# Kernel tuning notes

Hardware: AMD Instinct MI355X
Metric: run time of the kernel (lower is better)

## Reference

```python
import jax, jax.numpy as jnp
import numpy as np

B, CIN, COUT, DK, DV, NH, H, W = 8, 256, 512, 256, 256, 8, 32, 32
DKH = DK // NH  # 32
DVH = DV // NH  # 32


def _conv(x, w, b, pad):
    y = jax.lax.conv_general_dilated(
        x, w, window_strides=(1, 1), padding=[(pad, pad), (pad, pad)],
        dimension_numbers=('NCHW', 'OIHW', 'NCHW'))
    return y + b[None, :, None, None]


def setup_inputs() -> dict:
    key = jax.random.key(0)
    ks = jax.random.split(key, 6)
    s = jnp.float32(0.05)
    return {
        'x': jax.random.normal(ks[0], (B, CIN, H, W), jnp.float32),
        'w_conv': jax.random.normal(ks[1], (COUT - DV, CIN, 3, 3), jnp.float32) * s,
        'b_conv': jnp.zeros((COUT - DV,), jnp.float32),
        'w_qkv': jax.random.normal(ks[2], (2 * DK + DV, CIN, 3, 3), jnp.float32) * s,
        'b_qkv': jnp.zeros((2 * DK + DV,), jnp.float32),
        'w_att': jax.random.normal(ks[3], (DV, DV, 1, 1), jnp.float32) * s,
        'b_att': jnp.zeros((DV,), jnp.float32),
        'key_rel_w': jax.random.normal(ks[4], (2 * W - 1, DKH), jnp.float32),
        'key_rel_h': jax.random.normal(ks[5], (2 * H - 1, DKH), jnp.float32),
    }


def reference(x, w_conv, b_conv, w_qkv, b_qkv, w_att, b_att, key_rel_w, key_rel_h):
    qkv = _conv(x, w_qkv, b_qkv, 1)                 # (B, 2*DK+DV, H, W)
    b = x.shape[0]
    q, k, v = qkv[:, :DK], qkv[:, DK:2 * DK], qkv[:, 2 * DK:]
    q = q.reshape(b, NH, DKH, H, W) * (DKH ** -0.5)
    kf = k.reshape(b, NH, DKH, H * W)
    vf = v.reshape(b, NH, DVH, H * W)
    qf = q.reshape(b, NH, DKH, H * W)
    # content logits: (B, NH, HW, HW)
    logits = jnp.einsum('bhdm,bhdn->bhmn', qf, kf)
    # relative position logits (equivalent to the pad/reshape/slice skew trick)
    q5 = jnp.transpose(q, (0, 1, 3, 4, 2))          # (B, NH, H, W, DKH)
    rel_w = jnp.einsum('bhxyd,md->bhxym', q5, key_rel_w)   # (B,NH,H,W,2W-1)
    idx_w = (jnp.arange(W)[None, :] - jnp.arange(W)[:, None]) + (W - 1)  # idx[y,y']
    rel_w = jnp.take_along_axis(rel_w, idx_w[None, None, None], axis=-1)  # (B,NH,H,W,W) [x,y,y']
    rel_h = jnp.einsum('bhxyd,md->bhxym', q5, key_rel_h)   # (B,NH,H,W,2H-1)
    idx_h = (jnp.arange(H)[None, :] - jnp.arange(H)[:, None]) + (H - 1)  # idx[x,x']
    rel_h = jnp.take_along_axis(rel_h, idx_h[None, None, :, None, :], axis=-1)  # (B,NH,H,W,H) [x,y,x']
    # logits6 axes: [x, y, x', y']
    logits6 = (logits.reshape(b, NH, H, W, H, W)
               + rel_w[:, :, :, :, None, :]
               + rel_h[:, :, :, :, :, None])
    weights = jax.nn.softmax(logits6.reshape(b, NH, H * W, H * W), axis=-1)
    att = jnp.einsum('bhmn,bhdn->bhmd', weights, vf)  # (B, NH, HW, DVH)
    # faithful to torch's contiguous .view(batch, dim_v, H, W)
    att = att.reshape(b, DV, H, W)
    att = _conv(att, w_att, b_att, 0)
    xo = _conv(x, w_conv, b_conv, 1)
    return jnp.concatenate([xo, att], axis=1)
```

## Files before the change

kernel.cpp:

```cpp
#include <hip/hip_runtime.h>


typedef __attribute__((ext_vector_type(8))) short short8;
typedef __attribute__((ext_vector_type(4))) float floatx4;

__device__ __forceinline__ unsigned short f2bf(float f) {
    unsigned int u = __float_as_uint(f);
    u += 0x7FFFu + ((u >> 16) & 1u);
    return (unsigned short)(u >> 16);
}
__device__ __forceinline__ float bf2f(unsigned short s) {
    return __uint_as_float(((unsigned int)s) << 16);
}
__device__ __forceinline__ unsigned int pk2bf_trunc(float lo, float hi) {
    return (__float_as_uint(lo) >> 16) | (__float_as_uint(hi) & 0xFFFF0000u);
}
__device__ __forceinline__ unsigned int pk2bf_rne(float lo, float hi) {
    return (unsigned int)f2bf(lo) | ((unsigned int)f2bf(hi) << 16);
}
__device__ __forceinline__ void gload_lds16(const unsigned short* g, unsigned short* s) {
    __builtin_amdgcn_global_load_lds(
        (const __attribute__((address_space(1))) unsigned int*)g,
        (__attribute__((address_space(3))) unsigned int*)s, 16, 0, 0);
}

__global__ __launch_bounds__(256) void k_xt(const float* __restrict__ x,
                                            unsigned short* __restrict__ Xt) {
    __shared__ unsigned short lds[256 * 33];
    const int tid = threadIdx.x;
    const int yy = blockIdx.x % 34;
    const int b  = blockIdx.x / 34;
    unsigned int* outp = (unsigned int*)(Xt + (((size_t)b * 34 + yy) * 34) * 256);
    if (yy == 0 || yy == 33) {
        for (int i = tid; i < 4352; i += 256) outp[i] = 0;
        return;
    }
    const int y = yy - 1;
    const float* xb = x + (size_t)b * 262144 + y * 32;
#pragma unroll
    for (int it = 0; it < 32; ++it) {
        const int e = it * 256 + tid;
        const int ci = e >> 5, xx = e & 31;
        lds[ci * 33 + xx] = f2bf(xb[ci * 1024 + xx]);
    }
    __syncthreads();
    const int ci2 = (tid & 127) * 2;
    const int xh = tid >> 7;
#pragma unroll
    for (int it = 0; it < 17; ++it) {
        const int xx = xh * 17 + it;
        unsigned int v = 0;
        if (xx >= 1 && xx <= 32)
            v = (unsigned int)lds[ci2 * 33 + xx - 1] |
                ((unsigned int)lds[(ci2 + 1) * 33 + xx - 1] << 16);
        outp[xx * 128 + (tid & 127)] = v;
    }
}

__global__ __launch_bounds__(256) void k_wconv(const float* __restrict__ wc,
                                               const float* __restrict__ wq,
                                               const float* __restrict__ wa,
                                               const float* __restrict__ krw,
                                               const float* __restrict__ krh,
                                               unsigned short* __restrict__ wt,
                                               unsigned short* __restrict__ wt2,
                                               unsigned short* __restrict__ krwb,
                                               unsigned short* __restrict__ krhb) {
    const int tid = threadIdx.x;
    const int blk = blockIdx.x;
    if (blk < 1024) {
        __shared__ float lw[2304];
        const int n = blk;
        const float* src = (n < 256) ? (wc + (size_t)n * 2304)
                                     : (wq + (size_t)(n - 256) * 2304);
#pragma unroll
        for (int it = 0; it < 9; ++it)
            lw[it * 256 + tid] = src[it * 256 + tid];
        __syncthreads();
#pragma unroll
        for (int it = 0; it < 9; ++it) {
            const int kp = it * 256 + tid;
            const int g = kp >> 8, ci = kp & 255;
            wt[(size_t)n * 2304 + kp] = f2bf(lw[ci * 9 + g]);
        }
    } else {
        const int i = (blk - 1024) * 256 + tid;
        if (i < 65536)        wt2[i] = f2bf(wa[i]);
        else if (i < 67584) { const int j = i - 65536;
                              krwb[j] = (j < 2016) ? f2bf(krw[j]) : (unsigned short)0; }
        else if (i < 69632) { const int j = i - 67584;
                              krhb[j] = (j < 2016) ? f2bf(krh[j]) : (unsigned short)0; }
    }
}

__global__ __launch_bounds__(256, 4) void k_gemm0(const unsigned short* __restrict__ Wr,
                                                  const unsigned short* __restrict__ Xt,
                                                  float* __restrict__ out,
                                                  unsigned short* __restrict__ qT,
                                                  unsigned short* __restrict__ kT,
                                                  unsigned short* __restrict__ vT,
                                                  const float* __restrict__ bias_a,
                                                  const float* __restrict__ bias_b) {
    __shared__ unsigned short As[64 * 64];
    __shared__ unsigned short Bs[128 * 64];
    const int tid = threadIdx.x;
    const int lane = tid & 63, wv = tid >> 6;
    const int l15 = lane & 15, quad = lane >> 4;
    const int m0 = blockIdx.x * 128, n0 = blockIdx.y * 64;
    const int wave_m = (wv & 1) * 64, wave_n = (wv >> 1) * 32;
    floatx4 acc[2][4] = {};
    const int lr = lane >> 3;
    const int swz8 = ((lane & 7) ^ lr) * 8;
    const unsigned short* gA = Wr + (size_t)(n0 + wv * 16 + lr) * 2304 + swz8;
    int bb0[4];
#pragma unroll
    for (int r = 0; r < 4; ++r) {
        const int m = m0 + wv * 32 + r * 8 + lr;
        const int b = m >> 10, p = m & 1023, y = p >> 5, x = p & 31;
        bb0[r] = ((b * 34 + y) * 34 + x) * 256;
    }
    unsigned short* sA0 = As + wv * 1024;
    unsigned short* sB0 = Bs + wv * 2048;
    const int sw0 = ((quad)     ^ (l15 & 7)) * 8;
    const int sw1 = ((4 + quad) ^ (l15 & 7)) * 8;
    for (int k0 = 0; k0 < 2304; k0 += 64) {
        const int g = k0 >> 8;
        const int ci0 = k0 & 255;
        const int ky = g / 3, kx = g - ky * 3;
        const int offu = (ky * 34 + kx) * 256 + ci0 + swz8;
        __syncthreads();
        gload_lds16(gA + k0, sA0);
        gload_lds16(gA + (size_t)8 * 2304 + k0, sA0 + 512);
#pragma unroll
        for (int r = 0; r < 4; ++r)
            gload_lds16(Xt + bb0[r] + offu, sB0 + r * 512);
        __syncthreads();
#pragma unroll
        for (int h = 0; h < 2; ++h) {
            const int sw = h ? sw1 : sw0;
            short8 a[2], b[4];
#pragma unroll
            for (int i = 0; i < 2; ++i)
                a[i] = *reinterpret_cast<const short8*>(As + (wave_n + i * 16 + l15) * 64 + sw);
#pragma unroll
            for (int j = 0; j < 4; ++j)
                b[j] = *reinterpret_cast<const short8*>(Bs + (wave_m + j * 16 + l15) * 64 + sw);
#pragma unroll
            for (int i = 0; i < 2; ++i)
#pragma unroll
                for (int j = 0; j < 4; ++j)
                    acc[i][j] = __builtin_amdgcn_mfma_f32_16x16x32_bf16(a[i], b[j], acc[i][j], 0, 0, 0);
        }
    }
#pragma unroll
    for (int i = 0; i < 2; ++i)
#pragma unroll
        for (int jj = 0; jj < 4; ++jj)
#pragma unroll
            for (int rg = 0; rg < 4; ++rg) {
                const int n = n0 + wave_n + i * 16 + quad * 4 + rg;
                const int m = m0 + wave_m + jj * 16 + l15;
                const float v = acc[i][jj][rg];
                const int bb = m >> 10, p = m & 1023;
                if (n < 256) {
                    out[(size_t)bb * 524288 + (size_t)n * 1024 + p] = v + bias_a[n];
                } else {
                    const int c = n - 256;
                    const float vq = v + bias_b[c];
                    if (c < 256) {
                        const int h = c >> 5, d = c & 31;
                        qT[(((size_t)(bb * 8 + h)) * 1024 + p) * 32 + d] =
                            f2bf(vq * 0.17677669529663687f);
                    } else if (c < 512) {
                        const int c2 = c - 256;
                        const int h = c2 >> 5, d = c2 & 31;
                        kT[(((size_t)(bb * 8 + h)) * 1024 + p) * 32 + d] = f2bf(vq);
                    } else {
                        const int c2 = c - 512;
                        const int h = c2 >> 5, d = c2 & 31;
                        vT[(((size_t)(bb * 8 + h)) * 32 + d) * 1024 + p] = f2bf(vq);
                    }
                }
            }
}

__global__ __launch_bounds__(256, 4) void k_attn(const unsigned short* __restrict__ qT,
                                                 const unsigned short* __restrict__ kT,
                                                 const unsigned short* __restrict__ vT,
                                                 const unsigned short* __restrict__ krwb,
                                                 const unsigned short* __restrict__ krhb,
                                                 unsigned short* __restrict__ attT) {
    __shared__ float rh_s[64 * 68];
    __shared__ unsigned short Pw[4 * 1152];
    const int tid = threadIdx.x;
    const int lane = tid & 63, wv = tid >> 6;
    const int l15 = lane & 15, quad = lane >> 4;
    const int bid = blockIdx.x;
    const int qt = bid & 15;
    const int h = (bid >> 4) & 7;
    const int b = bid >> 7;
    const int bh = b * 8 + h;
    const unsigned short* qbase = qT + (size_t)bh * 32768;
    const unsigned short* kbase = kT + (size_t)bh * 32768;
    const unsigned short* vbase = vT + (size_t)bh * 32768;
    const int qloc = wv * 16 + l15;
    const int pq = qt * 64 + qloc;
    const int yq = pq >> 5, xq = pq & 31;

    const short8 qfrag = *reinterpret_cast<const short8*>(
        qbase + (size_t)pq * 32 + quad * 8);
    const floatx4 zero = {0.f, 0.f, 0.f, 0.f};
    unsigned short* pw = Pw + wv * 1152;

#pragma unroll
    for (int sub = 0; sub < 4; ++sub) {
        const short8 aw = *reinterpret_cast<const short8*>(krwb + (sub * 16 + l15) * 32 + quad * 8);
        const short8 ah = *reinterpret_cast<const short8*>(krhb + (sub * 16 + l15) * 32 + quad * 8);
        const floatx4 dw = __builtin_amdgcn_mfma_f32_16x16x32_bf16(aw, qfrag, zero, 0, 0, 0);
        const floatx4 dh = __builtin_amdgcn_mfma_f32_16x16x32_bf16(ah, qfrag, zero, 0, 0, 0);
        *reinterpret_cast<floatx4*>(rh_s + qloc * 68 + sub * 16 + quad * 4) = dh;
        uint2 uu;
        uu.x = pk2bf_rne(dw[0], dw[1]);
        uu.y = pk2bf_rne(dw[2], dw[3]);
        *reinterpret_cast<uint2*>(pw + l15 * 64 + sub * 16 + quad * 4) = uu;
    }
    float rwreg[8];
#pragma unroll
    for (int j = 0; j < 8; ++j) {
        const int xn = (j >> 2) * 16 + quad * 4 + (j & 3);
        rwreg[j] = bf2f(pw[l15 * 64 + xn - xq + 31]);
    }
    asm volatile("s_waitcnt lgkmcnt(0)" ::: "memory");

    const float* rhq = rh_s + qloc * 68 + 31 - yq;
    float lsum = 0.f;
    floatx4 O0 = zero, O1 = zero;

    short8 kf[4], vf[4];
#pragma unroll
    for (int sub = 0; sub < 4; ++sub)
        kf[sub] = *reinterpret_cast<const short8*>(
            kbase + (size_t)(sub * 16 + l15) * 32 + quad * 8);
#pragma unroll
    for (int n2 = 0; n2 < 2; ++n2) {
        vf[n2 * 2 + 0] = *reinterpret_cast<const short8*>(
            vbase + (size_t)l15 * 1024 + n2 * 32 + quad * 8);
        vf[n2 * 2 + 1] = *reinterpret_cast<const short8*>(
            vbase + (size_t)(16 + l15) * 1024 + n2 * 32 + quad * 8);
    }

#pragma unroll
    for (int nt = 0; nt < 16; ++nt) {
        const int n0 = nt * 64;
        const int n0n = (nt < 15) ? n0 + 64 : n0;
        floatx4 d[4];
#pragma unroll
        for (int sub = 0; sub < 4; ++sub)
            d[sub] = __builtin_amdgcn_mfma_f32_16x16x32_bf16(kf[sub], qfrag, zero, 0, 0, 0);
        short8 kfn[4], vfn[4];
#pragma unroll
        for (int sub = 0; sub < 4; ++sub)
            kfn[sub] = *reinterpret_cast<const short8*>(
                kbase + (size_t)(n0n + sub * 16 + l15) * 32 + quad * 8);
        const float rh0 = rhq[nt * 2];
        const float rh1 = rhq[nt * 2 + 1];
        float p[16];
#pragma unroll
        for (int sub = 0; sub < 4; ++sub) {
            const float rhv = (sub >> 1) ? rh1 : rh0;
#pragma unroll
            for (int r = 0; r < 4; ++r) {
                const float e = __expf(d[sub][r] + rwreg[(sub & 1) * 4 + r] + rhv);
                p[sub * 4 + r] = e;
                lsum += e;
            }
        }
#pragma unroll
        for (int sub = 0; sub < 4; ++sub) {
            uint2 uu;
            uu.x = pk2bf_trunc(p[sub * 4 + 0], p[sub * 4 + 1]);
            uu.y = pk2bf_trunc(p[sub * 4 + 2], p[sub * 4 + 3]);
            *reinterpret_cast<uint2*>(pw + l15 * 72 + sub * 16 + quad * 4) = uu;
        }
        asm volatile("s_waitcnt lgkmcnt(0)" ::: "memory");
#pragma unroll
        for (int n2 = 0; n2 < 2; ++n2) {
            const short8 pfrag = *reinterpret_cast<const short8*>(
                pw + l15 * 72 + n2 * 32 + quad * 8);
            O0 = __builtin_amdgcn_mfma_f32_16x16x32_bf16(vf[n2 * 2 + 0], pfrag, O0, 0, 0, 0);
            O1 = __builtin_amdgcn_mfma_f32_16x16x32_bf16(vf[n2 * 2 + 1], pfrag, O1, 0, 0, 0);
        }
#pragma unroll
        for (int n2 = 0; n2 < 2; ++n2) {
            vfn[n2 * 2 + 0] = *reinterpret_cast<const short8*>(
                vbase + (size_t)l15 * 1024 + n0n + n2 * 32 + quad * 8);
            vfn[n2 * 2 + 1] = *reinterpret_cast<const short8*>(
                vbase + (size_t)(16 + l15) * 1024 + n0n + n2 * 32 + quad * 8);
        }
#pragma unroll
        for (int i = 0; i < 4; ++i) { kf[i] = kfn[i]; vf[i] = vfn[i]; }
    }
    lsum += __shfl_xor(lsum, 16);
    lsum += __shfl_xor(lsum, 32);
    const float inv = 1.0f / lsum;
    unsigned short* ob = attT + ((size_t)(h * 32 + yq)) * 8192 + b * 1024 + xq * 32;
    uint2 o0, o1;
    o0.x = pk2bf_rne(O0[0] * inv, O0[1] * inv);
    o0.y = pk2bf_rne(O0[2] * inv, O0[3] * inv);
    o1.x = pk2bf_rne(O1[0] * inv, O1[1] * inv);
    o1.y = pk2bf_rne(O1[2] * inv, O1[3] * inv);
    *reinterpret_cast<uint2*>(ob + quad * 4) = o0;
    *reinterpret_cast<uint2*>(ob + 16 + quad * 4) = o1;
}

__global__ __launch_bounds__(256) void k_tr(const unsigned short* __restrict__ src,
                                            unsigned short* __restrict__ dst) {
    __shared__ unsigned short t[64 * 72];
    const int tid = threadIdx.x;
    const int m0 = (blockIdx.x & 127) * 64;
    const int k0 = (blockIdx.x >> 7) * 64;
#pragma unroll
    for (int i = 0; i < 2; ++i) {
        const int idx = i * 256 + tid;
        const int k = idx >> 3, c8 = (idx & 7) * 8;
        *reinterpret_cast<uint4*>(t + k * 72 + c8) =
            *reinterpret_cast<const uint4*>(src + (size_t)(k0 + k) * 8192 + m0 + c8);
    }
    __syncthreads();
#pragma unroll
    for (int i = 0; i < 2; ++i) {
        const int idx = i * 256 + tid;
        const int m = idx >> 3, c8 = (idx & 7) * 8;
        unsigned short v[8];
#pragma unroll
        for (int j = 0; j < 8; ++j) v[j] = t[(c8 + j) * 72 + m];
        *reinterpret_cast<uint4*>(dst + (size_t)(m0 + m) * 256 + k0 + c8) =
            *reinterpret_cast<uint4*>(v);
    }
}

__global__ __launch_bounds__(256) void k_gemm_s(const unsigned short* __restrict__ Wm,
                                                const unsigned short* __restrict__ Dm,
                                                float* __restrict__ out,
                                                const float* __restrict__ bias) {
    __shared__ unsigned short As[64 * 40];
    __shared__ unsigned short Bs[64 * 40];
    const int tid = threadIdx.x;
    const int m0 = blockIdx.x * 64, n0 = blockIdx.y * 64;
    const int lane = tid & 63;
    const int wv = tid >> 6;
    const int l15 = lane & 15, quad = lane >> 4;
    const int n_off = (wv & 1) * 32, m_off = (wv >> 1) * 32;
    floatx4 acc[2][2] = {};
    const int r = tid >> 2, c8 = (tid & 3) * 8;
    const unsigned short* gA = Wm + (size_t)(n0 + r) * 256 + c8;
    const unsigned short* gB = Dm + (size_t)(m0 + r) * 256 + c8;
    unsigned short* sA = As + r * 40 + c8;
    unsigned short* sB = Bs + r * 40 + c8;
    for (int k0 = 0; k0 < 256; k0 += 32) {
        __syncthreads();
        *reinterpret_cast<uint4*>(sA) = *reinterpret_cast<const uint4*>(gA + k0);
        *reinterpret_cast<uint4*>(sB) = *reinterpret_cast<const uint4*>(gB + k0);
        __syncthreads();
        const short8 a0 = *reinterpret_cast<const short8*>(As + (n_off +      l15) * 40 + quad * 8);
        const short8 a1 = *reinterpret_cast<const short8*>(As + (n_off + 16 + l15) * 40 + quad * 8);
        const short8 b0 = *reinterpret_cast<const short8*>(Bs + (m_off +      l15) * 40 + quad * 8);
        const short8 b1 = *reinterpret_cast<const short8*>(Bs + (m_off + 16 + l15) * 40 + quad * 8);
        acc[0][0] = __builtin_amdgcn_mfma_f32_16x16x32_bf16(a0, b0, acc[0][0], 0, 0, 0);
        acc[0][1] = __builtin_amdgcn_mfma_f32_16x16x32_bf16(a0, b1, acc[0][1], 0, 0, 0);
        acc[1][0] = __builtin_amdgcn_mfma_f32_16x16x32_bf16(a1, b0, acc[1][0], 0, 0, 0);
        acc[1][1] = __builtin_amdgcn_mfma_f32_16x16x32_bf16(a1, b1, acc[1][1], 0, 0, 0);
    }
#pragma unroll
    for (int i = 0; i < 2; ++i)
#pragma unroll
        for (int jj = 0; jj < 2; ++jj)
#pragma unroll
            for (int rg = 0; rg < 4; ++rg) {
                const int n = n0 + n_off + i * 16 + quad * 4 + rg;
                const int m = m0 + m_off + jj * 16 + l15;
                const int bb = m >> 10, p = m & 1023;
                out[(size_t)bb * 524288 + (size_t)(n + 256) * 1024 + p] =
                    acc[i][jj][rg] + bias[n];
            }
}

extern "C" void kernel_launch(void* const* d_in, const int* in_sizes, int n_in,
                              void* d_out, int out_size, void* d_ws, size_t ws_size,
                              hipStream_t stream) {
    const float* x      = (const float*)d_in[0];
    const float* w_conv = (const float*)d_in[1];
    const float* b_conv = (const float*)d_in[2];
    const float* w_qkv  = (const float*)d_in[3];
    const float* b_qkv  = (const float*)d_in[4];
    const float* w_att  = (const float*)d_in[5];
    const float* b_att  = (const float*)d_in[6];
    const float* krw    = (const float*)d_in[7];
    const float* krh    = (const float*)d_in[8];
    float* out = (float*)d_out;

    char* ws = (char*)d_ws;
    unsigned short* Xt    = (unsigned short*)(ws);
    unsigned short* wt    = (unsigned short*)(ws + 9470464);
    unsigned short* wt2   = (unsigned short*)(ws + 14189056);
    unsigned short* qT    = (unsigned short*)(ws + 14320128);
    unsigned short* kT    = (unsigned short*)(ws + 18514432);
    unsigned short* vT    = (unsigned short*)(ws + 22708736);
    unsigned short* attt  = (unsigned short*)(ws + 26903040);
    unsigned short* krwb  = (unsigned short*)(ws + 31097344);
    unsigned short* krhb  = (unsigned short*)(ws + 31101440);
    unsigned short* attTT = (unsigned short*)(ws + 31105536);

    k_xt<<<dim3(272), dim3(256), 0, stream>>>(x, Xt);
    k_wconv<<<dim3(1296), dim3(256), 0, stream>>>(w_conv, w_qkv, w_att, krw, krh,
                                                  wt, wt2, krwb, krhb);
    k_gemm0<<<dim3(64, 16), dim3(256), 0, stream>>>(wt, Xt, out, qT, kT, vT,
                                                    b_conv, b_qkv);
    k_attn<<<dim3(1024), dim3(256), 0, stream>>>(qT, kT, vT, krwb, krhb, attTT);
    k_tr<<<dim3(512), dim3(256), 0, stream>>>(attTT, attt);
    k_gemm_s<<<dim3(128, 4), dim3(256), 0, stream>>>(wt2, attt, out, b_att);
}
```

Baseline: 195.0 us.

## Software-pipeline attention loop with double-buffered P tile and reorder block mapping

Restructures the attention inner loop so the QK MFMA and softmax exponentials for tile nt+1 run while the PV MFMAs for tile nt execute. A second LDS buffer is used for the probability tile, and K fragments are now prefetched two tiles ahead. The aim is to hide the LDS write-to-read latency and the exp work behind matrix ops. Block indexing also changes so that consecutive blocks cover different batch-head pairs rather than query tiles of the same head, which alters L2 locality. The cost is more LDS and more live registers, which may reduce occupancy.

New measurement: 287.6 us. 1.47x slower.

```diff
diff --git a/kernel.cpp b/kernel.cpp
--- a/kernel.cpp
+++ b/kernel.cpp
@@ -191,15 +191,15 @@
                                                  const unsigned short* __restrict__ krhb,
                                                  unsigned short* __restrict__ attT) {
     __shared__ float rh_s[64 * 68];
-    __shared__ unsigned short Pw[4 * 1152];
+    __shared__ unsigned short Pw[8 * 1152];
     const int tid = threadIdx.x;
     const int lane = tid & 63, wv = tid >> 6;
     const int l15 = lane & 15, quad = lane >> 4;
     const int bid = blockIdx.x;
-    const int qt = bid & 15;
-    const int h = (bid >> 4) & 7;
-    const int b = bid >> 7;
-    const int bh = b * 8 + h;
+    const int bh = bid & 63;
+    const int qt = bid >> 6;
+    const int h = bh & 7;
+    const int b = bh >> 3;
     const unsigned short* qbase = qT + (size_t)bh * 32768;
     const unsigned short* kbase = kT + (size_t)bh * 32768;
     const unsigned short* vbase = vT + (size_t)bh * 32768;
@@ -210,7 +210,8 @@
     const short8 qfrag = *reinterpret_cast<const short8*>(
         qbase + (size_t)pq * 32 + quad * 8);
     const floatx4 zero = {0.f, 0.f, 0.f, 0.f};
-    unsigned short* pw = Pw + wv * 1152;
+    unsigned short* pw0 = Pw + wv * 1152;
+    unsigned short* pw1 = Pw + 4608 + wv * 1152;
 
 #pragma unroll
     for (int sub = 0; sub < 4; ++sub) {
@@ -222,13 +223,13 @@
         uint2 uu;
         uu.x = pk2bf_rne(dw[0], dw[1]);
         uu.y = pk2bf_rne(dw[2], dw[3]);
-        *reinterpret_cast<uint2*>(pw + l15 * 64 + sub * 16 + quad * 4) = uu;
+        *reinterpret_cast<uint2*>(pw0 + l15 * 64 + sub * 16 + quad * 4) = uu;
     }
     float rwreg[8];
 #pragma unroll
     for (int j = 0; j < 8; ++j) {
         const int xn = (j >> 2) * 16 + quad * 4 + (j & 3);
-        rwreg[j] = bf2f(pw[l15 * 64 + xn - xq + 31]);
+        rwreg[j] = bf2f(pw0[l15 * 64 + xn - xq + 31]);
     }
     asm volatile("s_waitcnt lgkmcnt(0)" ::: "memory");
 
@@ -248,57 +249,87 @@
         vf[n2 * 2 + 1] = *reinterpret_cast<const short8*>(
             vbase + (size_t)(16 + l15) * 1024 + n2 * 32 + quad * 8);
     }
-
-#pragma unroll
-    for (int nt = 0; nt < 16; ++nt) {
-        const int n0 = nt * 64;
-        const int n0n = (nt < 15) ? n0 + 64 : n0;
+    {
         floatx4 d[4];
 #pragma unroll
         for (int sub = 0; sub < 4; ++sub)
             d[sub] = __builtin_amdgcn_mfma_f32_16x16x32_bf16(kf[sub], qfrag, zero, 0, 0, 0);
-        short8 kfn[4], vfn[4];
-#pragma unroll
-        for (int sub = 0; sub < 4; ++sub)
-            kfn[sub] = *reinterpret_cast<const short8*>(
-                kbase + (size_t)(n0n + sub * 16 + l15) * 32 + quad * 8);
-        const float rh0 = rhq[nt * 2];
-        const float rh1 = rhq[nt * 2 + 1];
-        float p[16];
+        const float rh0 = rhq[0], rh1 = rhq[1];
 #pragma unroll
         for (int sub = 0; sub < 4; ++sub) {
             const float rhv = (sub >> 1) ? rh1 : rh0;
+            float p[4];
 #pragma unroll
             for (int r = 0; r < 4; ++r) {
-                const float e = __expf(d[sub][r] + rwreg[(sub & 1) * 4 + r] + rhv);
-                p[sub * 4 + r] = e;
-                lsum += e;
+                p[r] = __expf(d[sub][r] + rwreg[(sub & 1) * 4 + r] + rhv);
+                lsum += p[r];
             }
-        }
-#pragma unroll
-        for (int sub = 0; sub < 4; ++sub) {
             uint2 uu;
-            uu.x = pk2bf_trunc(p[sub * 4 + 0], p[sub * 4 + 1]);
-            uu.y = pk2bf_trunc(p[sub * 4 + 2], p[sub * 4 + 3]);
-            *reinterpret_cast<uint2*>(pw + l15 * 72 + sub * 16 + quad * 4) = uu;
+            uu.x = pk2bf_trunc(p[0], p[1]);
+            uu.y = pk2bf_trunc(p[2], p[3]);
+            *reinterpret_cast<uint2*>(pw0 + l15 * 72 + sub * 16 + quad * 4) = uu;
+        }
+#pragma unroll
+        for (int sub = 0; sub < 4; ++sub)
+            kf[sub] = *reinterpret_cast<const short8*>(
+                kbase + (size_t)(64 + sub * 16 + l15) * 32 + quad * 8);
+    }
+
+#pragma unroll
+    for (int nt = 0; nt < 16; ++nt) {
+        unsigned short* pwr = (nt & 1) ? pw1 : pw0;
+        unsigned short* pww = (nt & 1) ? pw0 : pw1;
+        floatx4 d[4];
+        if (nt < 15) {
+#pragma unroll
+            for (int sub = 0; sub < 4; ++sub)
+                d[sub] = __builtin_amdgcn_mfma_f32_16x16x32_bf16(kf[sub], qfrag, zero, 0, 0, 0);
         }
         asm volatile("s_waitcnt lgkmcnt(0)" ::: "memory");
-#pragma unroll
-        for (int n2 = 0; n2 < 2; ++n2) {
-            const short8 pfrag = *reinterpret_cast<const short8*>(
-                pw + l15 * 72 + n2 * 32 + quad * 8);
-            O0 = __builtin_amdgcn_mfma_f32_16x16x32_bf16(vf[n2 * 2 + 0], pfrag, O0, 0, 0, 0);
-            O1 = __builtin_amdgcn_mfma_f32_16x16x32_bf16(vf[n2 * 2 + 1], pfrag, O1, 0, 0, 0);
-        }
-#pragma unroll
-        for (int n2 = 0; n2 < 2; ++n2) {
-            vfn[n2 * 2 + 0] = *reinterpret_cast<const short8*>(
-                vbase + (size_t)l15 * 1024 + n0n + n2 * 32 + quad * 8);
-            vfn[n2 * 2 + 1] = *reinterpret_cast<const short8*>(
-                vbase + (size_t)(16 + l15) * 1024 + n0n + n2 * 32 + quad * 8);
-        }
-#pragma unroll
-        for (int i = 0; i < 4; ++i) { kf[i] = kfn[i]; vf[i] = vfn[i]; }
+        short8 pfrag[2];
+#pragma unroll
+        for (int n2 = 0; n2 < 2; ++n2)
+            pfrag[n2] = *reinterpret_cast<const short8*>(
+                pwr + l15 * 72 + n2 * 32 + quad * 8);
+        if (nt < 15) {
+            const float rh0 = rhq[(nt + 1) * 2], rh1 = rhq[(nt + 1) * 2 + 1];
+#pragma unroll
+            for (int sub = 0; sub < 4; ++sub) {
+                const float rhv = (sub >> 1) ? rh1 : rh0;
+                float p[4];
+#pragma unroll
+                for (int r = 0; r < 4; ++r) {
+                    p[r] = __expf(d[sub][r] + rwreg[(sub & 1) * 4 + r] + rhv);
+                    lsum += p[r];
+                }
+                uint2 uu;
+                uu.x = pk2bf_trunc(p[0], p[1]);
+                uu.y = pk2bf_trunc(p[2], p[3]);
+                *reinterpret_cast<uint2*>(pww + l15 * 72 + sub * 16 + quad * 4) = uu;
+            }
+        }
+        O0 = __builtin_amdgcn_mfma_f32_16x16x32_bf16(vf[0], pfrag[0], O0, 0, 0, 0);
+        O1 = __builtin_amdgcn_mfma_f32_16x16x32_bf16(vf[1], pfrag[0], O1, 0, 0, 0);
+        O0 = __builtin_amdgcn_mfma_f32_16x16x32_bf16(vf[2], pfrag[1], O0, 0, 0, 0);
+        O1 = __builtin_amdgcn_mfma_f32_16x16x32_bf16(vf[3], pfrag[1], O1, 0, 0, 0);
+        if (nt < 14) {
+            const int nk = (nt + 2) * 64;
+#pragma unroll
+            for (int sub = 0; sub < 4; ++sub)
+                kf[sub] = *reinterpret_cast<const short8*>(
+                    kbase + (size_t)(nk + sub * 16 + l15) * 32 + quad * 8);
+        }
+        if (nt < 15) {
+            const int nv = (nt + 1) * 64;
+            vf[0] = *reinterpret_cast<const short8*>(
+                vbase + (size_t)l15 * 1024 + nv + quad * 8);
+            vf[1] = *reinterpret_cast<const short8*>(
+                vbase + (size_t)(16 + l15) * 1024 + nv + quad * 8);
+            vf[2] = *reinterpret_cast<const short8*>(
+                vbase + (size_t)l15 * 1024 + nv + 32 + quad * 8);
+            vf[3] = *reinterpret_cast<const short8*>(
+                vbase + (size_t)(16 + l15) * 1024 + nv + 32 + quad * 8);
+        }
     }
     lsum += __shfl_xor(lsum, 16);
     lsum += __shfl_xor(lsum, 32);
```
